# Kernel optimization log

Hardware: AMD Instinct MI355X
Metric: run time of the kernel (lower is better)

## Reference

```python
import jax, jax.numpy as jnp
import numpy as np


def setup_inputs() -> dict:
    key = jax.random.key(0)
    ks = jax.random.split(key, 5)
    B, S, D, F = 4, 2048, 1024, 4096
    scale_w1 = 1.0 / np.sqrt(D)
    scale_w2 = 1.0 / np.sqrt(F)
    return {
        "hidden_states": jax.random.normal(ks[0], (B, S, D), dtype=jnp.float32),
        "W1": jax.random.normal(ks[1], (F, D), dtype=jnp.float32) * scale_w1,
        "b1": jax.random.normal(ks[2], (F,), dtype=jnp.float32) * 0.02,
        "W2": jax.random.normal(ks[3], (D, F), dtype=jnp.float32) * scale_w2,
        "b2": jax.random.normal(ks[4], (D,), dtype=jnp.float32) * 0.02,
    }


def _sigmoid_poly(h):
    # cubic polynomial sigmoid approximation: 0.5 + 0.25*h - 0.0208*h^3
    h2 = h * h
    h3 = h2 * h
    return 0.5 + 0.25 * h + (-0.0208) * h3


def reference(hidden_states, W1, b1, W2, b2):
    # secure linear projection == plain affine: x @ W.T + b
    h = jnp.einsum("bsd,fd->bsf", hidden_states, W1) + b1  # [B,S,F]
    sw = h * _sigmoid_poly(h)                               # swish via poly sigmoid
    out = jnp.einsum("bsf,df->bsd", sw, W2) + b2            # [B,S,D]
    return out
```

## Files before the change

kernel.cpp:

```cpp
#include <hip/hip_runtime.h>
#include <hip/hip_bf16.h>

typedef __bf16 bf16_t;
typedef __bf16 bf16x8 __attribute__((ext_vector_type(8)));
typedef float f32x16 __attribute__((ext_vector_type(16)));

__global__ __launch_bounds__(256) void cast3_f32_to_bf16(
    const float* __restrict__ a, bf16_t* __restrict__ ao, int na8,
    const float* __restrict__ b, bf16_t* __restrict__ bo, int nb8,
    const float* __restrict__ c, bf16_t* __restrict__ co, int nc8) {
  int i = blockIdx.x * blockDim.x + threadIdx.x;
  const float* in;
  bf16_t* out;
  int j;
  if (i < na8) {
    in = a; out = ao; j = i;
  } else if (i < na8 + nb8) {
    in = b; out = bo; j = i - na8;
  } else if (i < na8 + nb8 + nc8) {
    in = c; out = co; j = i - na8 - nb8;
  } else {
    return;
  }
  const float4* in4 = (const float4*)in;
  float4 f0 = in4[2 * j];
  float4 f1 = in4[2 * j + 1];
  bf16x8 o;
  o[0] = (bf16_t)f0.x; o[1] = (bf16_t)f0.y;
  o[2] = (bf16_t)f0.z; o[3] = (bf16_t)f0.w;
  o[4] = (bf16_t)f1.x; o[5] = (bf16_t)f1.y;
  o[6] = (bf16_t)f1.z; o[7] = (bf16_t)f1.w;
  ((bf16x8*)out)[j] = o;
}

__device__ __forceinline__ void gload_lds16(const bf16_t* g, bf16_t* l) {
  __builtin_amdgcn_global_load_lds(
      (const __attribute__((address_space(1))) void*)g,
      (__attribute__((address_space(3))) void*)l,
      16, 0, 0);
}

template <bool SWISH>
__global__ __launch_bounds__(256, 2) void gemm_bt(
    const bf16_t* __restrict__ A, const bf16_t* __restrict__ B,
    const float* __restrict__ bias, void* __restrict__ Cout,
    int M, int N, int K, int XW, int px, int py) {
  const int tid = threadIdx.x;
  const int wave = tid >> 6;
  const int lane = tid & 63;

  const int bid = blockIdx.x;
  const int xcd = bid & 7;
  const int idx = bid >> 3;
  const int cx = xcd % XW;
  const int cy = xcd / XW;
  const int bx = cx * px + idx % px;
  const int by = cy * py + idx / px;
  const int tileM = by << 8;
  const int tileN = bx << 7;

  __shared__ __align__(16) bf16_t sA[2 * 256 * 32];
  __shared__ __align__(16) bf16_t sB[2 * 128 * 32];

  const int srow = (wave << 4) + (lane >> 2);
  const int gchunk = (lane & 3) ^ ((lane >> 3) & 3);
  const bf16_t* gA = A + (size_t)(tileM + srow) * K + gchunk * 8;
  const bf16_t* gB = B + (size_t)(tileN + srow) * K + gchunk * 8;
  bf16_t* lA = sA + (size_t)(wave << 4) * 32;
  bf16_t* lB = sB + (size_t)(wave << 4) * 32;

  const int wr = wave >> 1, wc = wave & 1;
  const int frow = lane & 31;
  const int pbase = (((lane >> 5) ^ ((lane >> 1) & 3)) << 3);
  int offA[4], offB[2];
#pragma unroll
  for (int i = 0; i < 4; ++i)
    offA[i] = (wr * 128 + i * 32 + frow) * 32 + pbase;
#pragma unroll
  for (int j = 0; j < 2; ++j)
    offB[j] = (wc * 64 + j * 32 + frow) * 32 + pbase;

  f32x16 acc[4][2] = {};

  const int niter = K >> 5;

#pragma unroll
  for (int r = 0; r < 4; ++r)
    gload_lds16(gA + (size_t)(r * 64) * K, lA + r * 64 * 32);
#pragma unroll
  for (int r = 0; r < 2; ++r)
    gload_lds16(gB + (size_t)(r * 64) * K, lB + r * 64 * 32);

  for (int it = 0; it < niter; ++it) {
    __syncthreads();
    const int p = it & 1;
    if (it + 1 < niter) {
      const int kt = (it + 1) << 5;
      const int q = p ^ 1;
#pragma unroll
      for (int r = 0; r < 4; ++r)
        gload_lds16(gA + kt + (size_t)(r * 64) * K,
                    lA + q * (256 * 32) + r * 64 * 32);
#pragma unroll
      for (int r = 0; r < 2; ++r)
        gload_lds16(gB + kt + (size_t)(r * 64) * K,
                    lB + q * (128 * 32) + r * 64 * 32);
    }
    const bf16_t* bA = sA + p * (256 * 32);
    const bf16_t* bB = sB + p * (128 * 32);
#pragma unroll
    for (int s = 0; s < 2; ++s) {
      const int sx = s << 4;
      bf16x8 af[4], bg[2];
#pragma unroll
      for (int i = 0; i < 4; ++i)
        af[i] = *(const bf16x8*)(bA + (offA[i] ^ sx));
#pragma unroll
      for (int j = 0; j < 2; ++j)
        bg[j] = *(const bf16x8*)(bB + (offB[j] ^ sx));
#pragma unroll
      for (int i = 0; i < 4; ++i)
#pragma unroll
        for (int j = 0; j < 2; ++j)
          acc[i][j] = __builtin_amdgcn_mfma_f32_32x32x16_bf16(
              af[i], bg[j], acc[i][j], 0, 0, 0);
    }
  }

  const int halfsel = (lane >> 5) << 2;
#pragma unroll
  for (int i = 0; i < 4; ++i) {
    const int row0 = tileM + wr * 128 + i * 32 + halfsel;
#pragma unroll
    for (int j = 0; j < 2; ++j) {
      const int col = tileN + wc * 64 + j * 32 + (lane & 31);
      const float bv = bias[col];
#pragma unroll
      for (int r = 0; r < 16; ++r) {
        const int row = row0 + (r & 3) + ((r >> 2) << 3);
        float h = acc[i][j][r] + bv;
        if constexpr (SWISH) {
          float h3 = h * h * h;
          float sw = h * (0.5f + 0.25f * h - 0.0208f * h3);
          ((bf16_t*)Cout)[(size_t)row * N + col] = (bf16_t)sw;
        } else {
          ((float*)Cout)[(size_t)row * N + col] = h;
        }
      }
    }
  }
}

extern "C" void kernel_launch(void* const* d_in, const int* in_sizes, int n_in,
                              void* d_out, int out_size, void* d_ws,
                              size_t ws_size, hipStream_t stream) {
  const float* X  = (const float*)d_in[0];
  const float* W1 = (const float*)d_in[1];
  const float* b1 = (const float*)d_in[2];
  const float* W2 = (const float*)d_in[3];
  const float* b2 = (const float*)d_in[4];
  float* out = (float*)d_out;

  const int F = in_sizes[2];
  const int D = in_sizes[4];
  const int M = in_sizes[0] / D;

  bf16_t* Xb  = (bf16_t*)d_ws;
  bf16_t* W1b = Xb + (size_t)M * D;
  bf16_t* W2b = W1b + (size_t)F * D;
  bf16_t* SW  = W2b + (size_t)D * F;

  const int nX = (M * D) / 8, nW1 = (F * D) / 8, nW2 = (D * F) / 8;
  const int nTot = nX + nW1 + nW2;
  cast3_f32_to_bf16<<<(nTot + 255) / 256, 256, 0, stream>>>(
      X, Xb, nX, W1, W1b, nW1, W2, W2b, nW2);

  {
    const int gx = F / 128, gy = M / 256;
    const int XW = 2, XH = 4;
    const int px = gx / XW, py = gy / XH;
    gemm_bt<true><<<gx * gy, 256, 0, stream>>>(
        Xb, W1b, b1, (void*)SW, M, F, D, XW, px, py);
  }

  {
    const int gx = D / 128, gy = M / 256;
    const int XW = 1, XH = 8;
    const int px = gx / XW, py = gy / XH;
    gemm_bt<false><<<gx * gy, 256, 0, stream>>>(
        SW, W2b, b2, (void*)out, M, D, F, XW, px, py);
  }
}
```

Before: 301.1 us.

## Replace double-buffered K=32 LDS pipeline with single-buffered K=64 tiles

Shared-memory staging moves from two K=32 buffers with prefetch of the next tile to one K=64 buffer that is loaded, synchronized, consumed, then synchronized again. The LDS swizzle and the global-load mapping are reworked for 64-wide rows (8 chunks per row XORed with row index). The total LDS footprint stays the same, and halving the number of iterations halves the barrier count. In exchange, load/compute overlap within a block is lost, so the kernel relies on the two co-resident blocks per CU to hide global-load latency.

```diff
diff --git a/kernel.cpp b/kernel.cpp
--- a/kernel.cpp
+++ b/kernel.cpp
@@ -59,65 +59,48 @@
   const int tileM = by << 8;
   const int tileN = bx << 7;
 
-  __shared__ __align__(16) bf16_t sA[2 * 256 * 32];
-  __shared__ __align__(16) bf16_t sB[2 * 128 * 32];
+  __shared__ __align__(16) bf16_t sA[256 * 64];
+  __shared__ __align__(16) bf16_t sB[128 * 64];
 
-  const int srow = (wave << 4) + (lane >> 2);
-  const int gchunk = (lane & 3) ^ ((lane >> 3) & 3);
-  const bf16_t* gA = A + (size_t)(tileM + srow) * K + gchunk * 8;
-  const bf16_t* gB = B + (size_t)(tileN + srow) * K + gchunk * 8;
-  bf16_t* lA = sA + (size_t)(wave << 4) * 32;
-  bf16_t* lB = sB + (size_t)(wave << 4) * 32;
+  const int lrow = lane >> 3;
+  const int gch = ((lane & 7) ^ lrow) << 3;
+  const bf16_t* gA = A + (size_t)(tileM + (wave << 6) + lrow) * K + gch;
+  const bf16_t* gB = B + (size_t)(tileN + (wave << 5) + lrow) * K + gch;
+  bf16_t* lA = sA + (size_t)(wave << 6) * 64;
+  bf16_t* lB = sB + (size_t)(wave << 5) * 64;
 
   const int wr = wave >> 1, wc = wave & 1;
   const int frow = lane & 31;
-  const int pbase = (((lane >> 5) ^ ((lane >> 1) & 3)) << 3);
+  const int p0 = (((lane >> 5) ^ (lane & 7)) << 3);
   int offA[4], offB[2];
 #pragma unroll
   for (int i = 0; i < 4; ++i)
-    offA[i] = (wr * 128 + i * 32 + frow) * 32 + pbase;
+    offA[i] = (wr * 128 + i * 32 + frow) * 64 + p0;
 #pragma unroll
   for (int j = 0; j < 2; ++j)
-    offB[j] = (wc * 64 + j * 32 + frow) * 32 + pbase;
+    offB[j] = (wc * 64 + j * 32 + frow) * 64 + p0;
 
   f32x16 acc[4][2] = {};
 
-  const int niter = K >> 5;
+  for (int kt = 0; kt < K; kt += 64) {
+#pragma unroll
+    for (int r = 0; r < 8; ++r)
+      gload_lds16(gA + kt + (size_t)(r * 8) * K, lA + r * 8 * 64);
+#pragma unroll
+    for (int r = 0; r < 4; ++r)
+      gload_lds16(gB + kt + (size_t)(r * 8) * K, lB + r * 8 * 64);
+    __syncthreads();
 
 #pragma unroll
-  for (int r = 0; r < 4; ++r)
-    gload_lds16(gA + (size_t)(r * 64) * K, lA + r * 64 * 32);
-#pragma unroll
-  for (int r = 0; r < 2; ++r)
-    gload_lds16(gB + (size_t)(r * 64) * K, lB + r * 64 * 32);
-
-  for (int it = 0; it < niter; ++it) {
-    __syncthreads();
-    const int p = it & 1;
-    if (it + 1 < niter) {
-      const int kt = (it + 1) << 5;
-      const int q = p ^ 1;
-#pragma unroll
-      for (int r = 0; r < 4; ++r)
-        gload_lds16(gA + kt + (size_t)(r * 64) * K,
-                    lA + q * (256 * 32) + r * 64 * 32);
-#pragma unroll
-      for (int r = 0; r < 2; ++r)
-        gload_lds16(gB + kt + (size_t)(r * 64) * K,
-                    lB + q * (128 * 32) + r * 64 * 32);
-    }
-    const bf16_t* bA = sA + p * (256 * 32);
-    const bf16_t* bB = sB + p * (128 * 32);
-#pragma unroll
-    for (int s = 0; s < 2; ++s) {
+    for (int s = 0; s < 4; ++s) {
       const int sx = s << 4;
       bf16x8 af[4], bg[2];
 #pragma unroll
       for (int i = 0; i < 4; ++i)
-        af[i] = *(const bf16x8*)(bA + (offA[i] ^ sx));
+        af[i] = *(const bf16x8*)(sA + (offA[i] ^ sx));
 #pragma unroll
       for (int j = 0; j < 2; ++j)
-        bg[j] = *(const bf16x8*)(bB + (offB[j] ^ sx));
+        bg[j] = *(const bf16x8*)(sB + (offB[j] ^ sx));
 #pragma unroll
       for (int i = 0; i < 4; ++i)
 #pragma unroll
@@ -125,6 +108,7 @@
           acc[i][j] = __builtin_amdgcn_mfma_f32_32x32x16_bf16(
               af[i], bg[j], acc[i][j], 0, 0, 0);
     }
+    __syncthreads();
   }
 
   const int halfsel = (lane >> 5) << 2;
```

New measurement: 272.0 us. 1.11x faster.
